# Performance work log

Hardware: AMD Instinct MI355X
Metric: run time of the kernel (lower is better)

Reference implementation:

```python
import jax, jax.numpy as jnp
import numpy as np
import math

V, L, H, D, T_MAX, FF = 50257, 12, 12, 768, 1024, 3072
B, T = 2, 1024
HD = D // H


def layernorm(x, g, b, eps=1e-5):
    m = x.mean(-1, keepdims=True)
    v = ((x - m) ** 2).mean(-1, keepdims=True)
    return (x - m) / jnp.sqrt(v + eps) * g + b


def mgelu(x):
    # note: module uses 0.047715 (not the standard 0.044715)
    return 0.5 * x * (1.0 + jnp.tanh(math.sqrt(2.0 / math.pi) * (x + 0.047715 * x ** 3)))


def setup_inputs() -> dict:
    key = jax.random.key(0)
    ks = jax.random.split(key, 16)
    s = 0.02
    sr = 0.02 * (2 * L) ** -0.5  # residual-projection init per GPT2 paper
    inp = {
        "idx": jax.random.randint(ks[0], (B, T), 0, V),
        "targets": jax.random.randint(ks[1], (B, T), 0, V),
        "wte": jax.random.normal(ks[2], (V, D), jnp.float32) * s,
        "wpe": jax.random.normal(ks[3], (T_MAX, D), jnp.float32) * s,
        "ln1_g": jnp.ones((L, D), jnp.float32),
        "ln1_b": jnp.zeros((L, D), jnp.float32),
        "qkv_w": jax.random.normal(ks[4], (L, D, 3 * D), jnp.float32) * s,
        "qkv_b": jnp.zeros((L, 3 * D), jnp.float32),
        "po_w": jax.random.normal(ks[5], (L, D, D), jnp.float32) * sr,
        "po_b": jnp.zeros((L, D), jnp.float32),
        "ln2_g": jnp.ones((L, D), jnp.float32),
        "ln2_b": jnp.zeros((L, D), jnp.float32),
        "fc_w": jax.random.normal(ks[6], (L, D, FF), jnp.float32) * s,
        "fc_b": jnp.zeros((L, FF), jnp.float32),
        "pr_w": jax.random.normal(ks[7], (L, FF, D), jnp.float32) * sr,
        "pr_b": jnp.zeros((L, D), jnp.float32),
        "lnf_g": jnp.ones((D,), jnp.float32),
        "lnf_b": jnp.zeros((D,), jnp.float32),
        "lm_w": jax.random.normal(ks[8], (D, V), jnp.float32) * s,
    }
    return inp


def gpt_forward(idx, targets, wte, wpe, ln1_g, ln1_b, qkv_w, qkv_b, po_w, po_b,
                ln2_g, ln2_b, fc_w, fc_b, pr_w, pr_b, lnf_g, lnf_b, lm_w):
    Bt, Tt = idx.shape
    x = wte[idx] + wpe[:Tt]  # [B,T,D]
    causal = jnp.tril(jnp.ones((Tt, Tt), bool))
    scale = 1.0 / math.sqrt(HD)

    def block(x, p):
        g1, b1, wq, bq, wo, bo, g2, b2, wf, bf, wp, bp = p
        h = layernorm(x, g1, b1)
        qkv = h @ wq + bq  # [B,T,3D]
        q, k, v = jnp.split(qkv, 3, axis=-1)
        q = q.reshape(Bt, Tt, H, HD)
        k = k.reshape(Bt, Tt, H, HD)
        v = v.reshape(Bt, Tt, H, HD)
        att = jnp.einsum('bqhd,bkhd->bhqk', q, k) * scale
        att = jnp.where(causal, att, -jnp.inf)
        att = jax.nn.softmax(att, axis=-1)  # dropout = identity (eval)
        y = jnp.einsum('bhqk,bkhd->bqhd', att, v).reshape(Bt, Tt, D)
        x = x + y @ wo + bo
        h2 = layernorm(x, g2, b2)
        x = x + mgelu(h2 @ wf + bf) @ wp + bp
        return x, None

    x, _ = jax.lax.scan(block, x, (ln1_g, ln1_b, qkv_w, qkv_b, po_w, po_b,
                                   ln2_g, ln2_b, fc_w, fc_b, pr_w, pr_b))
    x = layernorm(x, lnf_g, lnf_b)
    logits = x @ lm_w  # [B,T,V]

    logp = jax.nn.log_softmax(logits, axis=-1)
    valid = targets >= 0  # ignore_index=-1
    tgt = jnp.where(valid, targets, 0)
    nll = -jnp.take_along_axis(logp, tgt[..., None], axis=-1)[..., 0]
    loss = (nll * valid).sum() / valid.sum()
    return logits, loss


def reference(idx, targets, wte, wpe, ln1_g, ln1_b, qkv_w, qkv_b, po_w, po_b,
              ln2_g, ln2_b, fc_w, fc_b, pr_w, pr_b, lnf_g, lnf_b, lm_w):
    return gpt_forward(idx, targets, wte, wpe, ln1_g, ln1_b, qkv_w, qkv_b, po_w, po_b,
                       ln2_g, ln2_b, fc_w, fc_b, pr_w, pr_b, lnf_g, lnf_b, lm_w)
```

## Files before the change

kernel.cpp:

```cpp
#include <hip/hip_runtime.h>
#include <hip/hip_bf16.h>
#include <math.h>

#define VOC 50257
#define NL 12
#define NH 12
#define DM 768
#define FF 3072
#define BB 2
#define TT 1024
#define MR (BB*TT)

typedef __attribute__((ext_vector_type(8))) short bf16x8;
typedef __attribute__((ext_vector_type(4))) float f32x4;

__device__ __forceinline__ float mgelu_f(float x) {
    return 0.5f*x*(1.f + tanhf(0.7978845608028654f*(x + 0.047715f*x*x*x)));
}

__device__ __forceinline__ unsigned short f2bf(float f) {
    __hip_bfloat16 h = __float2bfloat16(f);
    return *reinterpret_cast<unsigned short*>(&h);
}

#define GLDS(gptr, lptr) __builtin_amdgcn_global_load_lds( \
    (const __attribute__((address_space(1))) void*)(gptr), \
    (__attribute__((address_space(3))) void*)(lptr), 16, 0, 0)

__device__ __forceinline__ int xcd_work(int bid, int total) {
    int xcd = bid & 7;
    int seq = bid >> 3;
    int q = total >> 3, r = total & 7;
    int base = (xcd < r) ? xcd*(q+1) : r + xcd*q;
    return base + seq;
}

__global__ void embed_kernel(const int* __restrict__ idx, const float* __restrict__ wte,
                             const float* __restrict__ wpe, float* __restrict__ x) {
    int row = blockIdx.x;
    int t = row % TT;
    int tok = idx[row];
    for (int d = threadIdx.x; d < DM; d += blockDim.x)
        x[(size_t)row*DM + d] = wte[(size_t)tok*DM + d] + wpe[(size_t)t*DM + d];
}

__global__ __launch_bounds__(256) void ln_kernel(const float* __restrict__ x,
                          const float* __restrict__ g,
                          const float* __restrict__ b, __hip_bfloat16* __restrict__ out) {
    int row = blockIdx.x*4 + (threadIdx.x >> 6);
    int lane = threadIdx.x & 63;
    const float* xr = x + (size_t)row*DM;
    float vals[DM/64];
    float s = 0.f;
    #pragma unroll
    for (int i = 0; i < DM/64; i++) { vals[i] = xr[lane + i*64]; s += vals[i]; }
    #pragma unroll
    for (int off = 32; off > 0; off >>= 1) s += __shfl_xor(s, off);
    float mean = s * (1.0f/DM);
    float vs = 0.f;
    #pragma unroll
    for (int i = 0; i < DM/64; i++) { float d = vals[i]-mean; vs += d*d; }
    #pragma unroll
    for (int off = 32; off > 0; off >>= 1) vs += __shfl_xor(vs, off);
    float rstd = rsqrtf(vs * (1.0f/DM) + 1e-5f);
    #pragma unroll
    for (int i = 0; i < DM/64; i++) {
        int d = lane + i*64;
        out[(size_t)row*DM + d] = __float2bfloat16((vals[i]-mean)*rstd*g[d] + b[d]);
    }
}

struct TJob { const float* in; __hip_bfloat16* out; int R, C, cx, tile0; };

__device__ __forceinline__ void trans_one(const TJob& j, int t) {
    __shared__ float tile[32][33];
    int bx = t % j.cx, by = t / j.cx;
    int c0 = bx*32, r0 = by*32;
    int tx = threadIdx.x, ty = threadIdx.y;
    #pragma unroll
    for (int i = ty; i < 32; i += 8) {
        int r = r0 + i, c = c0 + tx;
        tile[i][tx] = (r < j.R && c < j.C) ? j.in[(size_t)r*j.C + c] : 0.f;
    }
    __syncthreads();
    #pragma unroll
    for (int i = ty; i < 32; i += 8) {
        int c = c0 + i, r = r0 + tx;
        if (c < j.C && r < j.R) j.out[(size_t)c*j.R + r] = __float2bfloat16(tile[tx][i]);
    }
}

__global__ void trans4_kernel(TJob j0, TJob j1, TJob j2, TJob j3) {
    int t = blockIdx.x;
    if (t >= j3.tile0)      trans_one(j3, t - j3.tile0);
    else if (t >= j2.tile0) trans_one(j2, t - j2.tile0);
    else if (t >= j1.tile0) trans_one(j1, t - j1.tile0);
    else                    trans_one(j0, t);
}

__global__ void trans1_kernel(TJob j0) { trans_one(j0, blockIdx.x); }

template<int MODE, int HALFM>
__global__ __launch_bounds__(256) void mfma_gemm_kernel(
        const __hip_bfloat16* __restrict__ A,
        const __hip_bfloat16* __restrict__ Wt,
        const float* __restrict__ bias,
        const float* __restrict__ res,
        void* __restrict__ Cout,
        __hip_bfloat16* __restrict__ vt,
        float* __restrict__ part,
        int M, int N, int K) {
    constexpr int BM = HALFM ? 64 : 128;
    constexpr int NF = HALFM ? 2 : 4;
    constexpr int ABM = BM*64;
    constexpr int SMEMB = 3*ABM + 3*8192;
    __shared__ __align__(16) char smem[SMEMB];
    char* As = smem;
    char* Bs = smem + 3*ABM;
    int tid = threadIdx.x;
    int lane = tid & 63, wid = tid >> 6;
    int kq = lane >> 4, lr = lane & 15;

    int nby = M / BM;
    int work = xcd_work(blockIdx.x, gridDim.x);
    int by = work % nby;
    int bx = work / nby;
    int m0 = by * BM, n0 = bx * 128;

    int wm = HALFM ? 0 : (wid >> 1);
    int wn = HALFM ? wid : (wid & 1);
    int colbase = HALFM ? wn*32 : wn*64;

    f32x4 acc[4][NF] = {};

    auto STAGE = [&](int slot, int k0) {
        if constexpr (HALFM) {
            GLDS(A + (size_t)(m0 + lane)*K + k0 + wid*8, As + slot*ABM + wid*1024);
            #pragma unroll
            for (int t = 0; t < 2; t++) {
                int lx = wid + t*4;
                int r  = (lx & 1)*64 + lane;
                int kk = (lx >> 1)*8;
                int nr = n0 + r; if (nr > N-1) nr = N-1;
                GLDS(Wt + (size_t)nr*K + k0 + kk, Bs + slot*8192 + lx*1024);
            }
        } else {
            #pragma unroll
            for (int t = 0; t < 2; t++) {
                int lx = wid + t*4;
                int r  = (lx & 1)*64 + lane;
                int kk = (lx >> 1)*8;
                GLDS(A + (size_t)(m0 + r)*K + k0 + kk, As + slot*ABM + lx*1024);
                int nr = n0 + r; if (nr > N-1) nr = N-1;
                GLDS(Wt + (size_t)nr*K + k0 + kk, Bs + slot*8192 + lx*1024);
            }
        }
    };

    int nk = K >> 5;
    STAGE(0, 0);
    STAGE(1, (1 < nk ? 1 : nk-1)*32);
    for (int ki = 0; ki < nk; ++ki) {
        int cur = ki % 3;
        int k2 = (ki+2 < nk ? ki+2 : nk-1)*32;
        STAGE((ki+2) % 3, k2);
        __builtin_amdgcn_sched_barrier(0);
        if constexpr (HALFM) asm volatile("s_waitcnt vmcnt(6)" ::: "memory");
        else                 asm volatile("s_waitcnt vmcnt(8)" ::: "memory");
        __builtin_amdgcn_s_barrier();
        __builtin_amdgcn_sched_barrier(0);

        bf16x8 afrag[4], bfrag[NF];
        #pragma unroll
        for (int m = 0; m < 4; m++)
            afrag[m] = *(const bf16x8*)(As + cur*ABM + kq*(BM*16) + (wm*64 + m*16 + lr)*16);
        #pragma unroll
        for (int n = 0; n < NF; n++)
            bfrag[n] = *(const bf16x8*)(Bs + cur*8192 + kq*2048 + (colbase + n*16 + lr)*16);
        #pragma unroll
        for (int m = 0; m < 4; m++)
            #pragma unroll
            for (int n = 0; n < NF; n++)
                acc[m][n] = __builtin_amdgcn_mfma_f32_16x16x32_bf16(afrag[m], bfrag[n], acc[m][n], 0, 0, 0);

        __builtin_amdgcn_sched_barrier(0);
        asm volatile("s_waitcnt lgkmcnt(0)" ::: "memory");
        __builtin_amdgcn_s_barrier();
    }

    if (MODE == 0) {
        float* eps = (float*)smem;
        int nbx = (N + 127) >> 7;
        int rl2 = tid >> 1, sub = tid & 1;
        float pm = -INFINITY, ps = 0.f;
        #pragma unroll
        for (int hh = 0; hh < 2; ++hh) {
            __syncthreads();
            if (wn == hh) {
                #pragma unroll
                for (int m = 0; m < 4; m++)
                    #pragma unroll
                    for (int n = 0; n < 4; n++) {
                        int cl = n*16 + lr;
                        #pragma unroll
                        for (int j = 0; j < 4; j++)
                            eps[(wm*64 + m*16 + kq*4 + j)*68 + cl] = acc[m][n][j];
                    }
            }
            __syncthreads();
            #pragma unroll
            for (int it = 0; it < 8; ++it) {
                int rl = it*16 + (tid >> 4);
                int c4 = tid & 15;
                int col = n0 + hh*64 + c4*4;
                int row = m0 + rl;
                f32x4 v = *(const f32x4*)(eps + rl*68 + c4*4);
                if (col + 3 < N) {
                    __builtin_nontemporal_store(v, (f32x4*)&((float*)Cout)[(size_t)row*N + col]);
                } else {
                    #pragma unroll
                    for (int u = 0; u < 4; ++u)
                        if (col + u < N)
                            __builtin_nontemporal_store(v[u], &((float*)Cout)[(size_t)row*N + col + u]);
                }
            }
            #pragma unroll
            for (int i = 0; i < 8; ++i) {
                f32x4 v = *(const f32x4*)(eps + rl2*68 + sub*32 + i*4);
                #pragma unroll
                for (int u = 0; u < 4; ++u) {
                    int col = n0 + hh*64 + sub*32 + i*4 + u;
                    float xv = (col < N) ? v[u] : -INFINITY;
                    if (xv > pm) { ps = ps*__expf(pm - xv); pm = xv; ps += 1.f; }
                    else ps += __expf(xv - pm);
                }
            }
        }
        float m2 = __shfl_xor(pm, 1), s2 = __shfl_xor(ps, 1);
        float Mx = fmaxf(pm, m2);
        float Sx = ps*__expf(pm - Mx) + s2*__expf(m2 - Mx);
        if (sub == 0)
            ((float2*)part)[(size_t)(m0 + rl2)*nbx + bx] = make_float2(Mx, Sx);
        return;
    }

    #pragma unroll
    for (int m = 0; m < 4; m++) {
        #pragma unroll
        for (int n = 0; n < NF; n++) {
            int col = n0 + colbase + n*16 + lr;
            if (col >= N) continue;
            float bv = bias[col];
            #pragma unroll
            for (int j = 0; j < 4; j++) {
                int row = m0 + wm*64 + m*16 + kq*4 + j;
                float v = acc[m][n][j] + bv;
                size_t o = (size_t)row*N + col;
                if (MODE == 1) {
                    __hip_bfloat16 bvv = __float2bfloat16(v);
                    ((__hip_bfloat16*)Cout)[o] = bvv;
                    if (col >= 2*DM) {
                        int hh = (col - 2*DM) >> 6, dd = (col - 2*DM) & 63;
                        int bb = row >> 10, tt = row & 1023;
                        vt[(((size_t)bb*NH + hh)*64 + dd)*TT + tt] = bvv;
                    }
                } else if (MODE == 2) {
                    ((float*)Cout)[o] = v + res[o];
                } else {
                    ((__hip_bfloat16*)Cout)[o] = __float2bfloat16(mgelu_f(v));
                }
            }
        }
    }
}

__global__ __launch_bounds__(256) void mfma_attn_kernel(const __hip_bfloat16* __restrict__ qkv,
                                                        const __hip_bfloat16* __restrict__ vt,
                                                        __hip_bfloat16* __restrict__ y) {
    __shared__ __align__(16) char K_lds[3][8192];
    __shared__ __align__(16) char VT_lds[3][8192];
    __shared__ __align__(16) char P_lds[4][2048];

    int work = xcd_work(blockIdx.x, BB*NH*16);
    int qt = 15 - (work & 15);
    int bh = work >> 4;
    int h  = bh % NH;
    int b  = bh / NH;
    int tid = threadIdx.x;
    int lane = tid & 63, w = tid >> 6;
    int lr = lane & 15, kq = lane >> 4;
    int q0 = qt * 64;

    int sr = lane >> 3;
    int scb = (lane & 7) * 16;

    int qrow = q0 + w*16 + lr;
    const __hip_bfloat16* qp = qkv + (size_t)(b*TT + qrow)*3*DM + h*64;
    bf16x8 qfrag[2];
    qfrag[0] = *(const bf16x8*)(qp + kq*8);
    qfrag[1] = *(const bf16x8*)(qp + 32 + kq*8);

    f32x4 oacc[4] = {};
    float m_run = -INFINITY, l_run = 0.f;
    const float scale = 0.125f;

    const char* kbase  = (const char*)qkv + ((size_t)b*TT*3*DM + DM + h*64)*2;
    const char* vtbase = (const char*)vt + ((size_t)(b*NH + h)*64)*TT*2;

    auto STAGE = [&](int slot, int kt) {
        int kv0 = kt*64;
        #pragma unroll
        for (int t = 0; t < 2; t++) {
            int lx = w + t*4;
            int r = lx*8 + sr;
            int cbs = scb ^ ((r & 7) << 4);
            GLDS(kbase + (size_t)(kv0 + r)*3*DM*2 + cbs, K_lds[slot] + lx*1024);
            GLDS(vtbase + (size_t)r*TT*2 + kv0*2 + cbs, VT_lds[slot] + lx*1024);
        }
    };

    STAGE(0, 0);
    STAGE(1, 1 <= qt ? 1 : qt);
    for (int kt = 0; kt <= qt; ++kt) {
        int cur = kt % 3;
        STAGE((kt+2) % 3, kt+2 <= qt ? kt+2 : qt);
        __builtin_amdgcn_sched_barrier(0);
        asm volatile("s_waitcnt vmcnt(8)" ::: "memory");
        __builtin_amdgcn_s_barrier();
        __builtin_amdgcn_sched_barrier(0);

        f32x4 st[4] = {};
        #pragma unroll
        for (int t = 0; t < 4; ++t) {
            #pragma unroll
            for (int ks = 0; ks < 2; ++ks) {
                int row = t*16 + lr;
                bf16x8 kf = *(const bf16x8*)(K_lds[cur] + row*128 + ((ks*64 + kq*16) ^ ((lr&7)<<4)));
                st[t] = __builtin_amdgcn_mfma_f32_16x16x32_bf16(kf, qfrag[ks], st[t], 0,0,0);
            }
        }

        float sv[4][4];
        bool diag = (kt == qt);
        float pmax = -INFINITY;
        #pragma unroll
        for (int t = 0; t < 4; ++t)
            #pragma unroll
            for (int jj = 0; jj < 4; ++jj) {
                float s = st[t][jj] * scale;
                if (diag && (t*16 + kq*4 + jj > w*16 + lr)) s = -INFINITY;
                sv[t][jj] = s;
                pmax = fmaxf(pmax, s);
            }
        pmax = fmaxf(pmax, __shfl_xor(pmax, 16));
        pmax = fmaxf(pmax, __shfl_xor(pmax, 32));
        float m_new = fmaxf(m_run, pmax);
        float corr = __expf(m_run - m_new);
        float rsum = 0.f;
        #pragma unroll
        for (int t = 0; t < 4; ++t)
            #pragma unroll
            for (int jj = 0; jj < 4; ++jj) {
                float p = __expf(sv[t][jj] - m_new);
                sv[t][jj] = p;
                rsum += p;
            }
        rsum += __shfl_xor(rsum, 16);
        rsum += __shfl_xor(rsum, 32);
        l_run = l_run * corr + rsum;
        m_run = m_new;

        #pragma unroll
        for (int jj = 0; jj < 4; ++jj) {
            float c = __shfl(corr, kq*20 + jj);
            #pragma unroll
            for (int nt = 0; nt < 4; ++nt) oacc[nt][jj] *= c;
        }

        #pragma unroll
        for (int t = 0; t < 4; ++t) {
            unsigned pk0 = (unsigned)f2bf(sv[t][0]) | ((unsigned)f2bf(sv[t][1]) << 16);
            unsigned pk1 = (unsigned)f2bf(sv[t][2]) | ((unsigned)f2bf(sv[t][3]) << 16);
            unsigned off = ((unsigned)(lr*128 + t*32 + kq*8)) ^ (((unsigned)lr&7u)<<4);
            *(uint2*)(P_lds[w] + off) = make_uint2(pk0, pk1);
        }

        #pragma unroll
        for (int ks = 0; ks < 2; ++ks) {
            bf16x8 pa = *(const bf16x8*)(P_lds[w] +
                ((unsigned)(lr*128 + ((ks*64 + kq*16) ^ ((lr&7)<<4)))));
            #pragma unroll
            for (int nt = 0; nt < 4; ++nt) {
                int row = nt*16 + lr;
                bf16x8 vf = *(const bf16x8*)(VT_lds[cur] + row*128 + ((ks*64 + kq*16) ^ ((lr&7)<<4)));
                oacc[nt] = __builtin_amdgcn_mfma_f32_16x16x32_bf16(pa, vf, oacc[nt], 0,0,0);
            }
        }

        __builtin_amdgcn_sched_barrier(0);
        asm volatile("s_waitcnt lgkmcnt(0)" ::: "memory");
        __builtin_amdgcn_s_barrier();
    }

    #pragma unroll
    for (int jj = 0; jj < 4; ++jj) {
        float li = __shfl(l_run, kq*20 + jj);
        int qg = q0 + w*16 + kq*4 + jj;
        #pragma unroll
        for (int nt = 0; nt < 4; ++nt)
            y[(size_t)(b*TT + qg)*DM + h*64 + nt*16 + lr] =
                __float2bfloat16(oacc[nt][jj] / li);
    }
}

__global__ void zero_acc_kernel(float* p) { p[threadIdx.x] = 0.f; }

__global__ __launch_bounds__(64) void loss_reduce_kernel(const float* __restrict__ part,
                                                         const float* __restrict__ logits,
                                                         const int* __restrict__ targets,
                                                         float* __restrict__ acc) {
    int row = blockIdx.x;
    int lane = threadIdx.x;
    const int nbx = (VOC + 127) >> 7;
    float m = -INFINITY, s = 0.f;
    for (int bx = lane; bx < nbx; bx += 64) {
        float2 p = ((const float2*)part)[(size_t)row*nbx + bx];
        float Mx = fmaxf(m, p.x);
        s = s*__expf(m - Mx) + p.y*__expf(p.x - Mx);
        m = Mx;
    }
    #pragma unroll
    for (int off = 32; off > 0; off >>= 1) {
        float m2 = __shfl_xor(m, off), s2 = __shfl_xor(s, off);
        float Mx = fmaxf(m, m2);
        s = s*__expf(m - Mx) + s2*__expf(m2 - Mx);
        m = Mx;
    }
    if (lane == 0) {
        int tgt = targets[row];
        if (tgt >= 0) {
            float lse = logf(s) + m;
            atomicAdd(&acc[0], lse - logits[(size_t)row*VOC + tgt]);
            atomicAdd(&acc[1], 1.f);
        }
    }
}

__global__ void loss_final_kernel(const float* acc, float* out) {
    out[0] = acc[0] / acc[1];
}

static inline TJob mkjob(const float* in, __hip_bfloat16* out, int R, int C, int tile0) {
    TJob j; j.in = in; j.out = out; j.R = R; j.C = C;
    j.cx = (C + 31)/32; j.tile0 = tile0;
    return j;
}

extern "C" void kernel_launch(void* const* d_in, const int* in_sizes, int n_in,
                              void* d_out, int out_size, void* d_ws, size_t ws_size,
                              hipStream_t stream) {
    const int*   idx     = (const int*)  d_in[0];
    const int*   targets = (const int*)  d_in[1];
    const float* wte     = (const float*)d_in[2];
    const float* wpe     = (const float*)d_in[3];
    const float* ln1_g   = (const float*)d_in[4];
    const float* ln1_b   = (const float*)d_in[5];
    const float* qkv_w   = (const float*)d_in[6];
    const float* qkv_b   = (const float*)d_in[7];
    const float* po_w    = (const float*)d_in[8];
    const float* po_b    = (const float*)d_in[9];
    const float* ln2_g   = (const float*)d_in[10];
    const float* ln2_b   = (const float*)d_in[11];
    const float* fc_w    = (const float*)d_in[12];
    const float* fc_b    = (const float*)d_in[13];
    const float* pr_w    = (const float*)d_in[14];
    const float* pr_b    = (const float*)d_in[15];
    const float* lnf_g   = (const float*)d_in[16];
    const float* lnf_b   = (const float*)d_in[17];
    const float* lm_w    = (const float*)d_in[18];

    float* logits = (float*)d_out;

    char* p = (char*)d_ws;
    float* x = (float*)p;                 p += (size_t)MR*DM*4;
    __hip_bfloat16* h    = (__hip_bfloat16*)p; p += (size_t)MR*DM*2;
    __hip_bfloat16* qkvb = (__hip_bfloat16*)p; p += (size_t)MR*3*DM*2;
    __hip_bfloat16* yb   = (__hip_bfloat16*)p; p += (size_t)MR*DM*2;
    __hip_bfloat16* fb   = (__hip_bfloat16*)p; p += (size_t)MR*FF*2;
    __hip_bfloat16* vtb  = (__hip_bfloat16*)p; p += (size_t)BB*NH*64*TT*2;
    __hip_bfloat16* lm_wt  = (__hip_bfloat16*)p; p += (size_t)VOC*DM*2;
    __hip_bfloat16* qkv_wt = (__hip_bfloat16*)p; p += (size_t)3*DM*DM*2;
    __hip_bfloat16* po_wt  = (__hip_bfloat16*)p; p += (size_t)DM*DM*2;
    __hip_bfloat16* fc_wt  = (__hip_bfloat16*)p; p += (size_t)FF*DM*2;
    __hip_bfloat16* pr_wt  = (__hip_bfloat16*)p; p += (size_t)DM*FF*2;
    float* part = (float*)p;              p += (size_t)MR*((VOC+127)/128)*2*4;
    float* lacc = (float*)p;

    dim3 tpb(32, 8);

    embed_kernel<<<MR, 256, 0, stream>>>(idx, wte, wpe, x);

    {
        TJob j = mkjob(lm_w, lm_wt, DM, VOC, 0);
        int tiles = j.cx * ((DM+31)/32);
        trans1_kernel<<<tiles, tpb, 0, stream>>>(j);
    }

    for (int l = 0; l < NL; l++) {
        TJob j0 = mkjob(qkv_w + (size_t)l*DM*3*DM, qkv_wt, DM, 3*DM, 0);
        int t1 = j0.cx * 24;
        TJob j1 = mkjob(po_w + (size_t)l*DM*DM, po_wt, DM, DM, t1);
        int t2 = t1 + j1.cx * 24;
        TJob j2 = mkjob(fc_w + (size_t)l*DM*FF, fc_wt, DM, FF, t2);
        int t3 = t2 + j2.cx * 24;
        TJob j3 = mkjob(pr_w + (size_t)l*FF*DM, pr_wt, FF, DM, t3);
        int tot = t3 + j3.cx * 96;
        trans4_kernel<<<tot, tpb, 0, stream>>>(j0, j1, j2, j3);

        ln_kernel<<<MR/4, 256, 0, stream>>>(x, ln1_g + l*DM, ln1_b + l*DM, h);
        mfma_gemm_kernel<1,0><<<(3*DM/128)*(MR/128), 256, 0, stream>>>(
            h, qkv_wt, qkv_b + (size_t)l*3*DM, nullptr, qkvb, vtb, nullptr, MR, 3*DM, DM);
        mfma_attn_kernel<<<BB*NH*(TT/64), 256, 0, stream>>>(qkvb, vtb, yb);
        mfma_gemm_kernel<2,1><<<(DM/128)*(MR/64), 256, 0, stream>>>(
            yb, po_wt, po_b + (size_t)l*DM, x, x, nullptr, nullptr, MR, DM, DM);
        ln_kernel<<<MR/4, 256, 0, stream>>>(x, ln2_g + l*DM, ln2_b + l*DM, h);
        mfma_gemm_kernel<3,0><<<(FF/128)*(MR/128), 256, 0, stream>>>(
            h, fc_wt, fc_b + (size_t)l*FF, nullptr, fb, nullptr, nullptr, MR, FF, DM);
        mfma_gemm_kernel<2,1><<<(DM/128)*(MR/64), 256, 0, stream>>>(
            fb, pr_wt, pr_b + (size_t)l*DM, x, x, nullptr, nullptr, MR, DM, FF);
    }

    ln_kernel<<<MR/4, 256, 0, stream>>>(x, lnf_g, lnf_b, h);
    mfma_gemm_kernel<0,0><<<((VOC+127)/128)*(MR/128), 256, 0, stream>>>(
        h, lm_wt, nullptr, nullptr, logits, nullptr, part, MR, VOC, DM);

    zero_acc_kernel<<<1, 2, 0, stream>>>(lacc);
    loss_reduce_kernel<<<MR, 64, 0, stream>>>(part, logits, targets, lacc);
    loss_final_kernel<<<1, 1, 0, stream>>>(lacc, logits + (size_t)MR*VOC);
}
```

Before: 2.868 ms.

## Use 128x256 tile with double-buffered ring for LM-head GEMM

```diff
diff --git a/kernel.cpp b/kernel.cpp
--- a/kernel.cpp
+++ b/kernel.cpp
@@ -100,7 +100,7 @@
 
 __global__ void trans1_kernel(TJob j0) { trans_one(j0, blockIdx.x); }
 
-template<int MODE, int HALFM>
+template<int MODE, int TILE>
 __global__ __launch_bounds__(256) void mfma_gemm_kernel(
         const __hip_bfloat16* __restrict__ A,
         const __hip_bfloat16* __restrict__ Wt,
@@ -110,13 +110,18 @@
         __hip_bfloat16* __restrict__ vt,
         float* __restrict__ part,
         int M, int N, int K) {
-    constexpr int BM = HALFM ? 64 : 128;
-    constexpr int NF = HALFM ? 2 : 4;
-    constexpr int ABM = BM*64;
-    constexpr int SMEMB = 3*ABM + 3*8192;
+    constexpr int BM    = (TILE == 1) ? 64 : 128;
+    constexpr int BN    = (TILE == 3) ? 256 : 128;
+    constexpr int MF    = 4;
+    constexpr int NF    = (TILE == 0) ? 4 : ((TILE == 3) ? 8 : 2);
+    constexpr int SLOTS = (TILE == 3) ? 2 : 3;
+    constexpr int ABM   = BM*64;
+    constexpr int BBM   = BN*64;
+    constexpr int RING  = SLOTS*(ABM + BBM);
+    constexpr int SMEMB = (MODE == 0 && RING < 34816) ? 34816 : RING;
     __shared__ __align__(16) char smem[SMEMB];
     char* As = smem;
-    char* Bs = smem + 3*ABM;
+    char* Bs = smem + SLOTS*ABM;
     int tid = threadIdx.x;
     int lane = tid & 63, wid = tid >> 6;
     int kq = lane >> 4, lr = lane & 15;
@@ -125,26 +130,16 @@
     int work = xcd_work(blockIdx.x, gridDim.x);
     int by = work % nby;
     int bx = work / nby;
-    int m0 = by * BM, n0 = bx * 128;
-
-    int wm = HALFM ? 0 : (wid >> 1);
-    int wn = HALFM ? wid : (wid & 1);
-    int colbase = HALFM ? wn*32 : wn*64;
-
-    f32x4 acc[4][NF] = {};
+    int m0 = by * BM, n0 = bx * BN;
+
+    int wm = (TILE == 1) ? 0 : (wid >> 1);
+    int wn = (TILE == 1) ? wid : (wid & 1);
+    int colbase = (TILE == 0) ? wn*64 : ((TILE == 3) ? wn*128 : wn*32);
+
+    f32x4 acc[MF][NF] = {};
 
     auto STAGE = [&](int slot, int k0) {
-        if constexpr (HALFM) {
-            GLDS(A + (size_t)(m0 + lane)*K + k0 + wid*8, As + slot*ABM + wid*1024);
-            #pragma unroll
-            for (int t = 0; t < 2; t++) {
-                int lx = wid + t*4;
-                int r  = (lx & 1)*64 + lane;
-                int kk = (lx >> 1)*8;
-                int nr = n0 + r; if (nr > N-1) nr = N-1;
-                GLDS(Wt + (size_t)nr*K + k0 + kk, Bs + slot*8192 + lx*1024);
-            }
-        } else {
+        if constexpr (TILE == 0) {
             #pragma unroll
             for (int t = 0; t < 2; t++) {
                 int lx = wid + t*4;
@@ -152,33 +147,60 @@
                 int kk = (lx >> 1)*8;
                 GLDS(A + (size_t)(m0 + r)*K + k0 + kk, As + slot*ABM + lx*1024);
                 int nr = n0 + r; if (nr > N-1) nr = N-1;
-                GLDS(Wt + (size_t)nr*K + k0 + kk, Bs + slot*8192 + lx*1024);
+                GLDS(Wt + (size_t)nr*K + k0 + kk, Bs + slot*BBM + lx*1024);
+            }
+        } else if constexpr (TILE == 1) {
+            GLDS(A + (size_t)(m0 + lane)*K + k0 + wid*8, As + slot*ABM + wid*1024);
+            #pragma unroll
+            for (int t = 0; t < 2; t++) {
+                int lx = wid + t*4;
+                int r  = (lx & 1)*64 + lane;
+                int kk = (lx >> 1)*8;
+                int nr = n0 + r; if (nr > N-1) nr = N-1;
+                GLDS(Wt + (size_t)nr*K + k0 + kk, Bs + slot*BBM + lx*1024);
+            }
+        } else {
+            #pragma unroll
+            for (int t = 0; t < 2; t++) {
+                int lx = wid + t*4;
+                int r  = (lx & 1)*64 + lane;
+                int kk = (lx >> 1)*8;
+                GLDS(A + (size_t)(m0 + r)*K + k0 + kk, As + slot*ABM + lx*1024);
+            }
+            #pragma unroll
+            for (int t = 0; t < 4; t++) {
+                int lx = wid + t*4;
+                int r  = (lx & 3)*64 + lane;
+                int kk = (lx >> 2)*8;
+                int nr = n0 + r; if (nr > N-1) nr = N-1;
+                GLDS(Wt + (size_t)nr*K + k0 + kk, Bs + slot*BBM + lx*1024);
             }
         }
     };
 
     int nk = K >> 5;
     STAGE(0, 0);
-    STAGE(1, (1 < nk ? 1 : nk-1)*32);
+    if constexpr (SLOTS == 3) STAGE(1, (1 < nk ? 1 : nk-1)*32);
     for (int ki = 0; ki < nk; ++ki) {
-        int cur = ki % 3;
-        int k2 = (ki+2 < nk ? ki+2 : nk-1)*32;
-        STAGE((ki+2) % 3, k2);
+        int cur = ki % SLOTS;
+        int ka = (ki+SLOTS-1 < nk ? ki+SLOTS-1 : nk-1)*32;
+        STAGE((ki+SLOTS-1) % SLOTS, ka);
         __builtin_amdgcn_sched_barrier(0);
-        if constexpr (HALFM) asm volatile("s_waitcnt vmcnt(6)" ::: "memory");
-        else                 asm volatile("s_waitcnt vmcnt(8)" ::: "memory");
+        if constexpr (TILE == 0)      asm volatile("s_waitcnt vmcnt(8)" ::: "memory");
+        else if constexpr (TILE == 1) asm volatile("s_waitcnt vmcnt(6)" ::: "memory");
+        else                          asm volatile("s_waitcnt vmcnt(6)" ::: "memory");
         __builtin_amdgcn_s_barrier();
         __builtin_amdgcn_sched_barrier(0);
 
-        bf16x8 afrag[4], bfrag[NF];
-        #pragma unroll
-        for (int m = 0; m < 4; m++)
+        bf16x8 afrag[MF], bfrag[NF];
+        #pragma unroll
+        for (int m = 0; m < MF; m++)
             afrag[m] = *(const bf16x8*)(As + cur*ABM + kq*(BM*16) + (wm*64 + m*16 + lr)*16);
         #pragma unroll
         for (int n = 0; n < NF; n++)
-            bfrag[n] = *(const bf16x8*)(Bs + cur*8192 + kq*2048 + (colbase + n*16 + lr)*16);
-        #pragma unroll
-        for (int m = 0; m < 4; m++)
+            bfrag[n] = *(const bf16x8*)(Bs + cur*BBM + kq*(BN*16) + (colbase + n*16 + lr)*16);
+        #pragma unroll
+        for (int m = 0; m < MF; m++)
             #pragma unroll
             for (int n = 0; n < NF; n++)
                 acc[m][n] = __builtin_amdgcn_mfma_f32_16x16x32_bf16(afrag[m], bfrag[n], acc[m][n], 0, 0, 0);
@@ -188,20 +210,21 @@
         __builtin_amdgcn_s_barrier();
     }
 
-    if (MODE == 0) {
+    if constexpr (MODE == 0) {
         float* eps = (float*)smem;
-        int nbx = (N + 127) >> 7;
+        int nbx = (N + 255) >> 8;
         int rl2 = tid >> 1, sub = tid & 1;
         float pm = -INFINITY, ps = 0.f;
         #pragma unroll
-        for (int hh = 0; hh < 2; ++hh) {
+        for (int s = 0; s < 4; ++s) {
             __syncthreads();
-            if (wn == hh) {
+            if (wn == (s >> 1)) {
                 #pragma unroll
                 for (int m = 0; m < 4; m++)
                     #pragma unroll
-                    for (int n = 0; n < 4; n++) {
-                        int cl = n*16 + lr;
+                    for (int nn = 0; nn < 4; nn++) {
+                        int n = (s & 1)*4 + nn;
+                        int cl = nn*16 + lr;
                         #pragma unroll
                         for (int j = 0; j < 4; j++)
                             eps[(wm*64 + m*16 + kq*4 + j)*68 + cl] = acc[m][n][j];
@@ -212,7 +235,7 @@
             for (int it = 0; it < 8; ++it) {
                 int rl = it*16 + (tid >> 4);
                 int c4 = tid & 15;
-                int col = n0 + hh*64 + c4*4;
+                int col = n0 + s*64 + c4*4;
                 int row = m0 + rl;
                 f32x4 v = *(const f32x4*)(eps + rl*68 + c4*4);
                 if (col + 3 < N) {
@@ -224,15 +247,26 @@
                             __builtin_nontemporal_store(v[u], &((float*)Cout)[(size_t)row*N + col + u]);
                 }
             }
+            float hm = -INFINITY;
             #pragma unroll
             for (int i = 0; i < 8; ++i) {
                 f32x4 v = *(const f32x4*)(eps + rl2*68 + sub*32 + i*4);
                 #pragma unroll
                 for (int u = 0; u < 4; ++u) {
-                    int col = n0 + hh*64 + sub*32 + i*4 + u;
-                    float xv = (col < N) ? v[u] : -INFINITY;
-                    if (xv > pm) { ps = ps*__expf(pm - xv); pm = xv; ps += 1.f; }
-                    else ps += __expf(xv - pm);
+                    int col = n0 + s*64 + sub*32 + i*4 + u;
+                    hm = fmaxf(hm, (col < N) ? v[u] : -INFINITY);
+                }
+            }
+            float nm = fmaxf(pm, hm);
+            ps *= __expf(pm - nm);
+            pm = nm;
+            #pragma unroll
+            for (int i = 0; i < 8; ++i) {
+                f32x4 v = *(const f32x4*)(eps + rl2*68 + sub*32 + i*4);
+                #pragma unroll
+                for (int u = 0; u < 4; ++u) {
+                    int col = n0 + s*64 + sub*32 + i*4 + u;
+                    ps += __expf(((col < N) ? v[u] : -INFINITY) - pm);
                 }
             }
         }
@@ -245,7 +279,7 @@
     }
 
     #pragma unroll
-    for (int m = 0; m < 4; m++) {
+    for (int m = 0; m < MF; m++) {
         #pragma unroll
         for (int n = 0; n < NF; n++) {
             int col = n0 + colbase + n*16 + lr;
@@ -421,7 +455,7 @@
                                                          float* __restrict__ acc) {
     int row = blockIdx.x;
     int lane = threadIdx.x;
-    const int nbx = (VOC + 127) >> 7;
+    const int nbx = (VOC + 255) >> 8;
     float m = -INFINITY, s = 0.f;
     for (int bx = lane; bx < nbx; bx += 64) {
         float2 p = ((const float2*)part)[(size_t)row*nbx + bx];
@@ -493,7 +527,7 @@
     __hip_bfloat16* po_wt  = (__hip_bfloat16*)p; p += (size_t)DM*DM*2;
     __hip_bfloat16* fc_wt  = (__hip_bfloat16*)p; p += (size_t)FF*DM*2;
     __hip_bfloat16* pr_wt  = (__hip_bfloat16*)p; p += (size_t)DM*FF*2;
-    float* part = (float*)p;              p += (size_t)MR*((VOC+127)/128)*2*4;
+    float* part = (float*)p;              p += (size_t)MR*((VOC+255)/256)*2*4;
     float* lacc = (float*)p;
 
     dim3 tpb(32, 8);
@@ -531,7 +565,7 @@
     }
 
     ln_kernel<<<MR/4, 256, 0, stream>>>(x, lnf_g, lnf_b, h);
-    mfma_gemm_kernel<0,0><<<((VOC+127)/128)*(MR/128), 256, 0, stream>>>(
+    mfma_gemm_kernel<0,3><<<((VOC+255)/256)*(MR/128), 256, 0, stream>>>(
         h, lm_wt, nullptr, nullptr, logits, nullptr, part, MR, VOC, DM);
 
     zero_acc_kernel<<<1, 2, 0, stream>>>(lacc);
```

After: 2.985 ms. 4.1% more time.
